# Performance work log

Measured on AMD Instinct MI355X. Metric: run time of the kernel, lower is better.

## Reference

```python
import jax, jax.numpy as jnp
import numpy as np

H, DN, DR, DV, L = 16, 128, 64, 128, 512
EPS = 1e-6

def rotate_half(x):
    x1, x2 = jnp.split(x, 2, axis=-1)
    return jnp.concatenate((-x2, x1), axis=-1)

def setup_inputs() -> dict:
    key = jax.random.key(0)
    ks = jax.random.split(key, 8)
    B, S, HID = 2, 2048, 2048
    inv_freq = 1.0 / (10000.0 ** (jnp.arange(0, DR, 2, dtype=jnp.float32) / DR))
    pos = jnp.arange(B * S, dtype=jnp.float32)
    freqs = pos[:, None] * inv_freq[None, :]
    emb = jnp.concatenate((freqs, freqs), axis=-1)
    return {
        "hidden_states": jax.random.normal(ks[0], (B, S, HID), jnp.float32),
        "cos": jnp.cos(emb),
        "sin": jnp.sin(emb),
        "q_proj_w": jax.random.normal(ks[1], (H * (DN + DR), HID), jnp.float32) * 0.02,
        "kv_a_proj_w": jax.random.normal(ks[2], (L + DR, HID), jnp.float32) * 0.02,
        "kv_a_ln_w": jnp.ones((L,), jnp.float32),
        "W_UK_T": jax.random.normal(ks[3], (H, DN, L), jnp.float32) * 0.02,
        "W_UV": jax.random.normal(ks[4], (H, L, DV), jnp.float32) * 0.02,
        "o_proj_w": jax.random.normal(ks[5], (HID, H * DV), jnp.float32) * 0.02,
    }

def reference(hidden_states, cos, sin, q_proj_w, kv_a_proj_w, kv_a_ln_w, W_UK_T, W_UV, o_proj_w):
    B, S, HID = hidden_states.shape
    T = B * S
    x = hidden_states.reshape(T, HID)
    # q projection -> [T, H, DN+DR]
    q = (x @ q_proj_w.T).reshape(T, H, DN + DR)
    q_pass, q_rot = q[..., :DN], q[..., DN:]
    # compressed kv -> latent + rope key (MQA-style, shared across heads)
    ckv = x @ kv_a_proj_w.T  # [T, L+DR]
    k_pass, k_rot = ckv[..., :L], ckv[..., L:]
    kv_c = k_pass * jax.lax.rsqrt(jnp.mean(k_pass * k_pass, axis=-1, keepdims=True) + EPS) * kv_a_ln_w
    # interleaved RoPE (rope_interleave=True): de-interleave then rotate_half form
    q_rot = q_rot.reshape(T, H, DR // 2, 2).swapaxes(-1, -2).reshape(T, H, DR)
    k_rot = k_rot.reshape(T, DR // 2, 2).swapaxes(-1, -2).reshape(T, DR)
    q_rot = q_rot * cos[:, None, :] + rotate_half(q_rot) * sin[:, None, :]
    k_rot = k_rot * cos + rotate_half(k_rot) * sin
    # absorb W_UK into queries: [T,H,L]
    q_lat = jnp.einsum('thd,hdl->thl', q_pass, W_UK_T)
    q_lat = q_lat.reshape(B, S, H, L)
    q_rot = q_rot.reshape(B, S, H, DR)
    kv_c_b = kv_c.reshape(B, S, L)
    k_rot_b = k_rot.reshape(B, S, DR)
    scale = 1.0 / np.sqrt(DN + DR)
    scores = (jnp.einsum('bshl,btl->bhst', q_lat, kv_c_b)
              + jnp.einsum('bshd,btd->bhst', q_rot, k_rot_b)) * scale
    causal = jnp.tril(jnp.ones((S, S), dtype=bool))
    scores = jnp.where(causal[None, None], scores, jnp.float32(-1e30))
    attn = jax.nn.softmax(scores, axis=-1)
    out_lat = jnp.einsum('bhst,btl->bshl', attn, kv_c_b)   # [B,S,H,L]
    out = jnp.einsum('bshl,hlv->bshv', out_lat, W_UV)       # [B,S,H,DV]
    out = out.reshape(B, S, H * DV) @ o_proj_w.T
    return out
```

## Files before the change

kernel.cpp:

```cpp
#include <hip/hip_runtime.h>
#include <stdint.h>

#define T_TOK 4096
#define HIDD  2048
#define NH    16
#define DNN   128
#define DRR   64
#define DVV   128
#define LAT   512
#define DQK   576
#define SEQ   2048
#define NB    2
#define KSTR  592
#define KCH   2368
#define QCKV  3712

typedef __attribute__((__ext_vector_type__(8))) short short8;
typedef __attribute__((__ext_vector_type__(4))) float f32x4;

__device__ __forceinline__ float bf2f(ushort u) {
  union { uint32_t i; float f; } v; v.i = ((uint32_t)u) << 16; return v.f;
}
__device__ __forceinline__ ushort f2bf(float f) {
  union { float f; uint32_t i; } v; v.f = f;
  uint32_t r = v.i + 0x7FFF + ((v.i >> 16) & 1);
  return (ushort)(r >> 16);
}

__device__ __forceinline__ void gld_lds16(const void* g, void* l) {
  __builtin_amdgcn_global_load_lds((const __attribute__((address_space(1))) void*)g,
                                   (__attribute__((address_space(3))) void*)l, 16, 0, 0);
}

__global__ void cast4(const float* __restrict__ in, ushort* __restrict__ out, int n4) {
  int i = blockIdx.x * blockDim.x + threadIdx.x;
  if (i >= n4) return;
  float4 v = ((const float4*)in)[i];
  ushort4 o; o.x = f2bf(v.x); o.y = f2bf(v.y); o.z = f2bf(v.z); o.w = f2bf(v.w);
  ((ushort4*)out)[i] = o;
}

__global__ void cast_pad_kv(const float* __restrict__ in, ushort* __restrict__ out) {
  int i = blockIdx.x * 256 + threadIdx.x;
  int row = (i * 4) >> 11;
  ushort4 o;
  if (row < 576) {
    float4 v = ((const float4*)in)[i];
    o.x = f2bf(v.x); o.y = f2bf(v.y); o.z = f2bf(v.z); o.w = f2bf(v.w);
  } else { o.x = 0; o.y = 0; o.z = 0; o.w = 0; }
  ((ushort4*)out)[i] = o;
}

__global__ void cast_wuk(const float* __restrict__ in, ushort* __restrict__ out) {
  int o = blockIdx.x * 256 + threadIdx.x;
  int d = o & 127, l = (o >> 7) & 511, h = o >> 16;
  out[o] = f2bf(in[((size_t)(h * 128 + d)) * 512 + l]);
}
__global__ void cast_wuv(const float* __restrict__ in, ushort* __restrict__ out) {
  int o = blockIdx.x * 256 + threadIdx.x;
  int l = o & 511, v = (o >> 9) & 127, h = o >> 16;
  out[o] = f2bf(in[((size_t)(h * 512 + l)) * 128 + v]);
}

template<int OUT_BF16>
__global__ __launch_bounds__(256) void gemm_bt(
    const ushort* __restrict__ A, const ushort* __restrict__ B, void* __restrict__ Cv,
    int K, int lda, int ldb, int ldc,
    long long aB, long long bB, long long cB)
{
  __shared__ ushort As[2][128 * 32];
  __shared__ ushort Bs[2][128 * 32];
  const int tid = threadIdx.x;
  const int lane = tid & 63, wid = tid >> 6;

  const int gx = gridDim.x;
  const int nwg = gx * gridDim.y;
  int l = blockIdx.y * gx + blockIdx.x;
  int tile = l;
  if ((nwg & 7) == 0) tile = (l & 7) * (nwg >> 3) + (l >> 3);
  const int m0 = (tile / gx) * 128, n0 = (tile % gx) * 128;

  A += (size_t)blockIdx.z * aB;
  B += (size_t)blockIdx.z * bB;
  const int wm = (wid >> 1) * 64, wn = (wid & 1) * 64;
  const int fr = lane & 15;
  const int kk = (lane >> 4) * 8;

  auto stage = [&](int k0, int buf) {
#pragma unroll
    for (int i = 0; i < 2; ++i) {
      int c = i * 256 + tid;
      gld_lds16(A + (size_t)(m0 + (c >> 2)) * lda + k0 + (c & 3) * 8, (void*)(&As[buf][0] + c * 8));
    }
#pragma unroll
    for (int i = 0; i < 2; ++i) {
      int c = i * 256 + tid;
      gld_lds16(B + (size_t)(n0 + (c >> 2)) * ldb + k0 + (c & 3) * 8, (void*)(&Bs[buf][0] + c * 8));
    }
  };

  f32x4 acc[4][4] = {};
  const int nt = K >> 5;
  stage(0, 0);
  for (int t = 0; t < nt; ++t) {
    const int cur = t & 1;
    if (t + 1 < nt) {
      stage((t + 1) << 5, cur ^ 1);
      asm volatile("s_waitcnt vmcnt(4)" ::: "memory");
    } else {
      asm volatile("s_waitcnt vmcnt(0)" ::: "memory");
    }
    __builtin_amdgcn_sched_barrier(0);
    __builtin_amdgcn_s_barrier();
    __builtin_amdgcn_sched_barrier(0);

    short8 af[4], bf[4];
#pragma unroll
    for (int x = 0; x < 4; ++x) af[x] = *(const short8*)(&As[cur][0] + (wm + x * 16 + fr) * 32 + kk);
#pragma unroll
    for (int x = 0; x < 4; ++x) bf[x] = *(const short8*)(&Bs[cur][0] + (wn + x * 16 + fr) * 32 + kk);
#pragma unroll
    for (int mi = 0; mi < 4; ++mi)
#pragma unroll
      for (int ni = 0; ni < 4; ++ni)
        acc[mi][ni] = __builtin_amdgcn_mfma_f32_16x16x32_bf16(af[mi], bf[ni], acc[mi][ni], 0, 0, 0);

    __builtin_amdgcn_sched_barrier(0);
    __builtin_amdgcn_s_barrier();
    __builtin_amdgcn_sched_barrier(0);
  }

  const int rb = (lane >> 4) * 4;
#pragma unroll
  for (int mi = 0; mi < 4; ++mi)
#pragma unroll
    for (int ni = 0; ni < 4; ++ni)
#pragma unroll
      for (int r = 0; r < 4; ++r) {
        size_t row = (size_t)(m0 + wm + mi * 16 + rb + r);
        size_t col = (size_t)(n0 + wn + ni * 16 + fr);
        size_t idx = row * (size_t)ldc + col + (size_t)blockIdx.z * cB;
        if (OUT_BF16) ((ushort*)Cv)[idx] = f2bf(acc[mi][ni][r]);
        else          ((float*)Cv)[idx]  = acc[mi][ni][r];
      }
}

__global__ __launch_bounds__(256) void rms_rope_k(
    const ushort* __restrict__ qckv, const float* __restrict__ lnw,
    const float* __restrict__ cosb, const float* __restrict__ sinb,
    ushort* __restrict__ k_eff)
{
  const int t = blockIdx.x, tid = threadIdx.x;
  __shared__ float red[4];
  const size_t base = (size_t)t * QCKV + 3072;
  float v0 = bf2f(qckv[base + tid]);
  float v1 = bf2f(qckv[base + 256 + tid]);
  float ss = v0 * v0 + v1 * v1;
#pragma unroll
  for (int m = 1; m < 64; m <<= 1) ss += __shfl_xor(ss, m);
  if ((tid & 63) == 0) red[tid >> 6] = ss;
  __syncthreads();
  float rn = rsqrtf((red[0] + red[1] + red[2] + red[3]) * (1.0f / 512.0f) + 1e-6f);
  k_eff[(size_t)t * KSTR + tid]       = f2bf(v0 * rn * lnw[tid]);
  k_eff[(size_t)t * KSTR + 256 + tid] = f2bf(v1 * rn * lnw[256 + tid]);
  if (tid < 64) {
    int j = tid;
    int src  = (j < 32) ? 2 * j : 2 * (j - 32) + 1;
    int psrc = (j < 32) ? src + 1 : src - 1;
    float xv = bf2f(qckv[base + 512 + src]);
    float pv = bf2f(qckv[base + 512 + psrc]);
    float c = cosb[t * 64 + j], s = sinb[t * 64 + j];
    k_eff[(size_t)t * KSTR + 512 + j] = f2bf((j < 32) ? xv * c - pv * s : xv * c + pv * s);
  }
}

__global__ __launch_bounds__(256) void transpose_kv(
    const ushort* __restrict__ keff, ushort* __restrict__ kvT)
{
  __shared__ ushort Tl[64][72];
  const int s0 = blockIdx.x * 64, v0 = blockIdx.y * 64, b = blockIdx.z;
  const int tid = threadIdx.x;
#pragma unroll
  for (int i = 0; i < 2; ++i) {
    int c = i * 256 + tid;
    int r = c >> 3, c8 = (c & 7) * 8;
    *(short8*)&Tl[r][c8] = *(const short8*)&keff[((size_t)b * SEQ + s0 + r) * KSTR + v0 + c8];
  }
  __syncthreads();
#pragma unroll
  for (int i = 0; i < 2; ++i) {
    int c = i * 256 + tid;
    int v = c >> 3, s8 = (c & 7) * 8;
    short8 o;
#pragma unroll
    for (int e = 0; e < 8; ++e) o[e] = Tl[s8 + e][v];
    *(short8*)&kvT[((size_t)b * 512 + v0 + v) * SEQ + s0 + s8] = o;
  }
}

__global__ void rope_q(const ushort* __restrict__ qb, const float* __restrict__ cosb,
                       const float* __restrict__ sinb, ushort* __restrict__ q_eff)
{
  const int t = blockIdx.x;
  const int h = blockIdx.y * 4 + threadIdx.y;
  const int j = threadIdx.x;
  size_t base = (size_t)t * QCKV + h * 192 + 128;
  int src  = (j < 32) ? 2 * j : 2 * (j - 32) + 1;
  int psrc = (j < 32) ? src + 1 : src - 1;
  float xv = bf2f(qb[base + src]), pv = bf2f(qb[base + psrc]);
  float c = cosb[t * 64 + j], s = sinb[t * 64 + j];
  q_eff[((size_t)h * T_TOK + t) * DQK + 512 + j] = f2bf((j < 32) ? xv * c - pv * s : xv * c + pv * s);
}

__global__ __launch_bounds__(512, 2) void attn3(
    const ushort* __restrict__ q_eff, const ushort* __restrict__ keff,
    const ushort* __restrict__ kvT, ushort* __restrict__ out_lat)
{
  const int pair = blockIdx.x;
  const int h = blockIdx.y, b = blockIdx.z;
  const int tid = threadIdx.x, lane = tid & 63, w = tid >> 6;
  __shared__ ushort Ks[2][32 * KSTR];
  __shared__ ushort Vt[2][512 * 32];
  __shared__ ushort Pl[8][16 * 40];

  const int fr = lane & 15, g = lane >> 4;

  auto stageK = [&](int kt, int buf) {
    const ushort* ksrc = keff + ((size_t)b * SEQ + (size_t)kt * 32) * KSTR;
    ushort* kd = &Ks[buf][0];
#pragma unroll
    for (int i = 0; i < 5; ++i) {
      int c0 = w * 320 + i * 64;
      if (c0 < KCH) {
        int c = c0 + lane;
        gld_lds16(ksrc + (size_t)c * 8, (void*)(kd + (size_t)c * 8));
      }
    }
  };
  auto stageV = [&](int kt, int buf) {
    const ushort* vsrc = kvT + (size_t)b * 512 * SEQ + (size_t)kt * 32;
    ushort* vd = &Vt[buf][0];
#pragma unroll
    for (int i = 0; i < 4; ++i) {
      int c = w * 256 + i * 64 + lane;
      gld_lds16(vsrc + (size_t)(c >> 2) * SEQ + (c & 3) * 8, (void*)(vd + (size_t)c * 8));
    }
  };

  for (int half = 0; half < 2; ++half) {
    const int qb = half ? pair : (15 - pair);
    const int q0 = qb * 128 + w * 16;

    const ushort* qrow = q_eff + ((size_t)h * T_TOK + (size_t)b * SEQ + q0 + fr) * DQK + g * 8;
    short8 qf[18];
#pragma unroll
    for (int ks = 0; ks < 18; ++ks) qf[ks] = *(const short8*)(qrow + ks * 32);

    f32x4 acc[32] = {};
    float m_s[4] = {-1e30f, -1e30f, -1e30f, -1e30f};
    float l_s[4] = {0.f, 0.f, 0.f, 0.f};

    const int nt = 4 * qb + 4;

    stageK(0, 0);
    stageV(0, 0);

    for (int kt = 0; kt < nt; ++kt) {
      const int cur = kt & 1;
      if (kt + 1 < nt) {
        stageK(kt + 1, cur ^ 1);
        stageV(kt + 1, cur ^ 1);
        if (w == 7) asm volatile("s_waitcnt vmcnt(6)" ::: "memory");
        else        asm volatile("s_waitcnt vmcnt(9)" ::: "memory");
      } else {
        asm volatile("s_waitcnt vmcnt(0)" ::: "memory");
      }
      __builtin_amdgcn_sched_barrier(0);
      __builtin_amdgcn_s_barrier();
      __builtin_amdgcn_sched_barrier(0);

      if (kt * 32 <= q0 + 15) {
        const ushort* Kc = &Ks[cur][0];
        const ushort* Vc = &Vt[cur][0];
        f32x4 s0 = {}, s1 = {};
        __builtin_amdgcn_s_setprio(1);
#pragma unroll
        for (int ks = 0; ks < 18; ++ks) {
          short8 b0 = *(const short8*)(Kc + (0 * 16 + fr) * KSTR + ks * 32 + g * 8);
          short8 b1 = *(const short8*)(Kc + (1 * 16 + fr) * KSTR + ks * 32 + g * 8);
          s0 = __builtin_amdgcn_mfma_f32_16x16x32_bf16(qf[ks], b0, s0, 0, 0, 0);
          s1 = __builtin_amdgcn_mfma_f32_16x16x32_bf16(qf[ks], b1, s1, 0, 0, 0);
        }
        __builtin_amdgcn_s_setprio(0);
        const float SC = 0.07216878364870322f;
        const bool diag = (kt * 32 + 31 > q0);
        float sv0[4], sv1[4];
#pragma unroll
        for (int r = 0; r < 4; ++r) {
          int qg = q0 + 4 * g + r;
          float a0 = s0[r] * SC, a1 = s1[r] * SC;
          if (diag) {
            if (kt * 32 + fr > qg)      a0 = -1e30f;
            if (kt * 32 + 16 + fr > qg) a1 = -1e30f;
          }
          sv0[r] = a0; sv1[r] = a1;
        }
        float mx[4];
#pragma unroll
        for (int r = 0; r < 4; ++r) {
          float m2 = fmaxf(sv0[r], sv1[r]);
          m2 = fmaxf(m2, __shfl_xor(m2, 1));
          m2 = fmaxf(m2, __shfl_xor(m2, 2));
          m2 = fmaxf(m2, __shfl_xor(m2, 4));
          m2 = fmaxf(m2, __shfl_xor(m2, 8));
          mx[r] = m2;
        }
        float need = mx[0] - m_s[0];
#pragma unroll
        for (int r = 1; r < 4; ++r) need = fmaxf(need, mx[r] - m_s[r]);
        if (__any(need > 8.0f)) {
          float rsc[4];
#pragma unroll
          for (int r = 0; r < 4; ++r) {
            float mn = fmaxf(m_s[r], mx[r]);
            rsc[r] = __expf(m_s[r] - mn);
            m_s[r] = mn;
            l_s[r] *= rsc[r];
          }
#pragma unroll
          for (int n2 = 0; n2 < 32; ++n2)
#pragma unroll
            for (int r = 0; r < 4; ++r) acc[n2][r] *= rsc[r];
        }
        float p0[4], p1[4];
#pragma unroll
        for (int r = 0; r < 4; ++r) {
          p0[r] = __expf(sv0[r] - m_s[r]);
          p1[r] = __expf(sv1[r] - m_s[r]);
          float ps = p0[r] + p1[r];
          ps += __shfl_xor(ps, 1);
          ps += __shfl_xor(ps, 2);
          ps += __shfl_xor(ps, 4);
          ps += __shfl_xor(ps, 8);
          l_s[r] += ps;
          Pl[w][(4 * g + r) * 40 + fr]      = f2bf(p0[r]);
          Pl[w][(4 * g + r) * 40 + 16 + fr] = f2bf(p1[r]);
        }
        short8 pa = *(const short8*)(Pl[w] + fr * 40 + g * 8);
        __builtin_amdgcn_s_setprio(1);
#pragma unroll
        for (int n2 = 0; n2 < 32; ++n2) {
          short8 bv = *(const short8*)(Vc + (n2 * 16 + fr) * 32 + g * 8);
          acc[n2] = __builtin_amdgcn_mfma_f32_16x16x32_bf16(pa, bv, acc[n2], 0, 0, 0);
        }
        __builtin_amdgcn_s_setprio(0);
      }
      __builtin_amdgcn_sched_barrier(0);
      __builtin_amdgcn_s_barrier();
      __builtin_amdgcn_sched_barrier(0);
    }

    const size_t obase = ((size_t)h * T_TOK + (size_t)b * SEQ + q0) * LAT;
    float inv[4];
#pragma unroll
    for (int r = 0; r < 4; ++r) inv[r] = 1.0f / l_s[r];
#pragma unroll
    for (int n2 = 0; n2 < 32; ++n2)
#pragma unroll
      for (int r = 0; r < 4; ++r)
        out_lat[obase + (size_t)(4 * g + r) * LAT + n2 * 16 + fr] = f2bf(acc[n2][r] * inv[r]);
  }
}

extern "C" void kernel_launch(void* const* d_in, const int* in_sizes, int n_in,
                              void* d_out, int out_size, void* d_ws, size_t ws_size,
                              hipStream_t stream) {
  const float* hs   = (const float*)d_in[0];
  const float* cosb = (const float*)d_in[1];
  const float* sinb = (const float*)d_in[2];
  const float* qw   = (const float*)d_in[3];
  const float* kvw  = (const float*)d_in[4];
  const float* lnw  = (const float*)d_in[5];
  const float* wuk  = (const float*)d_in[6];
  const float* wuv  = (const float*)d_in[7];
  const float* wo   = (const float*)d_in[8];
  float* out = (float*)d_out;
  char* ws = (char*)d_ws;

  const size_t o_xb   = 0;
  const size_t o_qb   = 16777216;
  const size_t o_wq   = 47185920;
  const size_t o_wkv  = 59768832;
  const size_t o_ol   = 0;
  const size_t o_wukt = 67108864;
  const size_t o_wuvt = 69206016;
  const size_t o_wo   = 71303168;
  const size_t o_keff = 79691776;
  const size_t o_qeff = 84541440;
  const size_t o_oh   = 160038912;
  const size_t o_kvt  = 176816128;

  ushort* xb    = (ushort*)(ws + o_xb);
  ushort* qbuf  = (ushort*)(ws + o_qb);
  ushort* wq_b  = (ushort*)(ws + o_wq);
  ushort* wkv_b = (ushort*)(ws + o_wkv);
  ushort* olat  = (ushort*)(ws + o_ol);
  ushort* wukt  = (ushort*)(ws + o_wukt);
  ushort* wuvt  = (ushort*)(ws + o_wuvt);
  ushort* wo_b  = (ushort*)(ws + o_wo);
  ushort* keff  = (ushort*)(ws + o_keff);
  ushort* qeff  = (ushort*)(ws + o_qeff);
  ushort* ohead = (ushort*)(ws + o_oh);
  ushort* kvt   = (ushort*)(ws + o_kvt);

  cast4<<<8192, 256, 0, stream>>>(hs, xb, 8388608 / 4);
  cast4<<<6144, 256, 0, stream>>>(qw, wq_b, 6291456 / 4);
  cast_pad_kv<<<1280, 256, 0, stream>>>(kvw, wkv_b);
  cast4<<<4096, 256, 0, stream>>>(wo, wo_b, 4194304 / 4);
  cast_wuk<<<4096, 256, 0, stream>>>(wuk, wukt);
  cast_wuv<<<4096, 256, 0, stream>>>(wuv, wuvt);

  gemm_bt<1><<<dim3(29, 32, 1), 256, 0, stream>>>(xb, wq_b, qbuf, 2048, 2048, 2048, QCKV, 0, 0, 0);
  rms_rope_k<<<4096, 256, 0, stream>>>(qbuf, lnw, cosb, sinb, keff);
  transpose_kv<<<dim3(32, 8, 2), 256, 0, stream>>>(keff, kvt);
  rope_q<<<dim3(4096, 4, 1), dim3(64, 4, 1), 0, stream>>>(qbuf, cosb, sinb, qeff);
  gemm_bt<1><<<dim3(4, 32, 16), 256, 0, stream>>>(qbuf, wukt, qeff, 128, QCKV, 128, 576,
                                                  192LL, 65536LL, 2359296LL);
  attn3<<<dim3(8, 16, 2), 512, 0, stream>>>(qeff, keff, kvt, olat);
  gemm_bt<1><<<dim3(1, 32, 16), 256, 0, stream>>>(olat, wuvt, ohead, 512, 512, 512, 2048,
                                                  2097152LL, 65536LL, 128LL);
  gemm_bt<0><<<dim3(16, 32, 1), 256, 0, stream>>>(ohead, wo_b, out, 2048, 2048, 2048, 2048, 0, 0, 0);
}
```

Baseline: 625.5 us.

## Shrink attention tiles to 64 query rows and 16-key steps with 16x16x16 MFMA

The causal latent-attention kernel now uses 256-thread blocks that each cover 64 query rows instead of 128, and steps through keys 16 at a time instead of 32. This doubles the grid and halves shared memory per block. The P·V product switches to 16x16x16 bf16 MFMA, with a fallback macro chain, so it matches the 16-key tile. The aim is better occupancy and finer causal skipping, paid for with more K/V reloads, twice as many barriers per key, and a smaller K dimension per MFMA; staging also over-reads some padding past each 16-row K tile.

```diff
diff --git a/kernel.cpp b/kernel.cpp
--- a/kernel.cpp
+++ b/kernel.cpp
@@ -12,11 +12,23 @@
 #define SEQ   2048
 #define NB    2
 #define KSTR  592
-#define KCH   2368
 #define QCKV  3712
 
 typedef __attribute__((__ext_vector_type__(8))) short short8;
+typedef __attribute__((__ext_vector_type__(4))) short short4v;
 typedef __attribute__((__ext_vector_type__(4))) float f32x4;
+
+#if __has_builtin(__builtin_amdgcn_mfma_f32_16x16x16_bf16)
+#define MFMA16(a, b, c) __builtin_amdgcn_mfma_f32_16x16x16_bf16(a, b, c, 0, 0, 0)
+#elif __has_builtin(__builtin_amdgcn_mfma_f32_16x16x16bf16_1k)
+#define MFMA16(a, b, c) __builtin_amdgcn_mfma_f32_16x16x16bf16_1k(a, b, c, 0, 0, 0)
+#else
+__device__ __forceinline__ f32x4 mfma16_asm(short4v a, short4v b, f32x4 c) {
+  asm volatile("v_mfma_f32_16x16x16_bf16 %0, %1, %2, %0" : "+v"(c) : "v"(a), "v"(b));
+  return c;
+}
+#define MFMA16(a, b, c) mfma16_asm(a, b, c)
+#endif
 
 __device__ __forceinline__ float bf2f(ushort u) {
   union { uint32_t i; float f; } v; v.i = ((uint32_t)u) << 16; return v.f;
@@ -212,44 +224,41 @@
   q_eff[((size_t)h * T_TOK + t) * DQK + 512 + j] = f2bf((j < 32) ? xv * c - pv * s : xv * c + pv * s);
 }
 
-__global__ __launch_bounds__(512, 2) void attn3(
+__global__ __launch_bounds__(256, 2) void attn7(
     const ushort* __restrict__ q_eff, const ushort* __restrict__ keff,
     const ushort* __restrict__ kvT, ushort* __restrict__ out_lat)
 {
   const int pair = blockIdx.x;
   const int h = blockIdx.y, b = blockIdx.z;
   const int tid = threadIdx.x, lane = tid & 63, w = tid >> 6;
-  __shared__ ushort Ks[2][32 * KSTR];
-  __shared__ ushort Vt[2][512 * 32];
-  __shared__ ushort Pl[8][16 * 40];
+  __shared__ ushort Ks[2][16 * 640];
+  __shared__ ushort Vt[2][512 * 16];
+  __shared__ ushort Pl[4][16 * 24];
 
   const int fr = lane & 15, g = lane >> 4;
 
   auto stageK = [&](int kt, int buf) {
-    const ushort* ksrc = keff + ((size_t)b * SEQ + (size_t)kt * 32) * KSTR;
+    const ushort* ksrc = keff + ((size_t)b * SEQ + (size_t)kt * 16) * KSTR;
     ushort* kd = &Ks[buf][0];
 #pragma unroll
     for (int i = 0; i < 5; ++i) {
-      int c0 = w * 320 + i * 64;
-      if (c0 < KCH) {
-        int c = c0 + lane;
-        gld_lds16(ksrc + (size_t)c * 8, (void*)(kd + (size_t)c * 8));
-      }
+      int c = i * 256 + tid;
+      gld_lds16(ksrc + (size_t)c * 8, (void*)(kd + (size_t)c * 8));
     }
   };
   auto stageV = [&](int kt, int buf) {
-    const ushort* vsrc = kvT + (size_t)b * 512 * SEQ + (size_t)kt * 32;
+    const ushort* vsrc = kvT + (size_t)b * 512 * SEQ + (size_t)kt * 16;
     ushort* vd = &Vt[buf][0];
 #pragma unroll
     for (int i = 0; i < 4; ++i) {
-      int c = w * 256 + i * 64 + lane;
-      gld_lds16(vsrc + (size_t)(c >> 2) * SEQ + (c & 3) * 8, (void*)(vd + (size_t)c * 8));
+      int c = i * 256 + tid;
+      gld_lds16(vsrc + (size_t)(c >> 1) * SEQ + (c & 1) * 8, (void*)(vd + (size_t)c * 8));
     }
   };
 
   for (int half = 0; half < 2; ++half) {
-    const int qb = half ? pair : (15 - pair);
-    const int q0 = qb * 128 + w * 16;
+    const int qb = half ? pair : (31 - pair);
+    const int q0 = qb * 64 + w * 16;
 
     const ushort* qrow = q_eff + ((size_t)h * T_TOK + (size_t)b * SEQ + q0 + fr) * DQK + g * 8;
     short8 qf[18];
@@ -270,8 +279,7 @@
       if (kt + 1 < nt) {
         stageK(kt + 1, cur ^ 1);
         stageV(kt + 1, cur ^ 1);
-        if (w == 7) asm volatile("s_waitcnt vmcnt(6)" ::: "memory");
-        else        asm volatile("s_waitcnt vmcnt(9)" ::: "memory");
+        asm volatile("s_waitcnt vmcnt(9)" ::: "memory");
       } else {
         asm volatile("s_waitcnt vmcnt(0)" ::: "memory");
       }
@@ -279,36 +287,31 @@
       __builtin_amdgcn_s_barrier();
       __builtin_amdgcn_sched_barrier(0);
 
-      if (kt * 32 <= q0 + 15) {
+      if (kt * 16 <= q0 + 15) {
         const ushort* Kc = &Ks[cur][0];
         const ushort* Vc = &Vt[cur][0];
-        f32x4 s0 = {}, s1 = {};
+        f32x4 s0 = {};
         __builtin_amdgcn_s_setprio(1);
 #pragma unroll
         for (int ks = 0; ks < 18; ++ks) {
-          short8 b0 = *(const short8*)(Kc + (0 * 16 + fr) * KSTR + ks * 32 + g * 8);
-          short8 b1 = *(const short8*)(Kc + (1 * 16 + fr) * KSTR + ks * 32 + g * 8);
+          short8 b0 = *(const short8*)(Kc + fr * KSTR + ks * 32 + g * 8);
           s0 = __builtin_amdgcn_mfma_f32_16x16x32_bf16(qf[ks], b0, s0, 0, 0, 0);
-          s1 = __builtin_amdgcn_mfma_f32_16x16x32_bf16(qf[ks], b1, s1, 0, 0, 0);
         }
         __builtin_amdgcn_s_setprio(0);
         const float SC = 0.07216878364870322f;
-        const bool diag = (kt * 32 + 31 > q0);
-        float sv0[4], sv1[4];
+        const bool diag = (kt * 16 + 15 > q0);
+        float sv0[4];
 #pragma unroll
         for (int r = 0; r < 4; ++r) {
           int qg = q0 + 4 * g + r;
-          float a0 = s0[r] * SC, a1 = s1[r] * SC;
-          if (diag) {
-            if (kt * 32 + fr > qg)      a0 = -1e30f;
-            if (kt * 32 + 16 + fr > qg) a1 = -1e30f;
-          }
-          sv0[r] = a0; sv1[r] = a1;
+          float a0 = s0[r] * SC;
+          if (diag && (kt * 16 + fr > qg)) a0 = -1e30f;
+          sv0[r] = a0;
         }
         float mx[4];
 #pragma unroll
         for (int r = 0; r < 4; ++r) {
-          float m2 = fmaxf(sv0[r], sv1[r]);
+          float m2 = sv0[r];
           m2 = fmaxf(m2, __shfl_xor(m2, 1));
           m2 = fmaxf(m2, __shfl_xor(m2, 2));
           m2 = fmaxf(m2, __shfl_xor(m2, 4));
@@ -332,26 +335,24 @@
 #pragma unroll
             for (int r = 0; r < 4; ++r) acc[n2][r] *= rsc[r];
         }
-        float p0[4], p1[4];
+        float p0[4];
 #pragma unroll
         for (int r = 0; r < 4; ++r) {
           p0[r] = __expf(sv0[r] - m_s[r]);
-          p1[r] = __expf(sv1[r] - m_s[r]);
-          float ps = p0[r] + p1[r];
+          float ps = p0[r];
           ps += __shfl_xor(ps, 1);
           ps += __shfl_xor(ps, 2);
           ps += __shfl_xor(ps, 4);
           ps += __shfl_xor(ps, 8);
           l_s[r] += ps;
-          Pl[w][(4 * g + r) * 40 + fr]      = f2bf(p0[r]);
-          Pl[w][(4 * g + r) * 40 + 16 + fr] = f2bf(p1[r]);
-        }
-        short8 pa = *(const short8*)(Pl[w] + fr * 40 + g * 8);
+          Pl[w][(4 * g + r) * 24 + fr] = f2bf(p0[r]);
+        }
+        short4v pa = *(const short4v*)(Pl[w] + fr * 24 + g * 4);
         __builtin_amdgcn_s_setprio(1);
 #pragma unroll
         for (int n2 = 0; n2 < 32; ++n2) {
-          short8 bv = *(const short8*)(Vc + (n2 * 16 + fr) * 32 + g * 8);
-          acc[n2] = __builtin_amdgcn_mfma_f32_16x16x32_bf16(pa, bv, acc[n2], 0, 0, 0);
+          short4v bv = *(const short4v*)(Vc + (n2 * 16 + fr) * 16 + g * 4);
+          acc[n2] = MFMA16(pa, bv, acc[n2]);
         }
         __builtin_amdgcn_s_setprio(0);
       }
@@ -426,7 +427,7 @@
   rope_q<<<dim3(4096, 4, 1), dim3(64, 4, 1), 0, stream>>>(qbuf, cosb, sinb, qeff);
   gemm_bt<1><<<dim3(4, 32, 16), 256, 0, stream>>>(qbuf, wukt, qeff, 128, QCKV, 128, 576,
                                                   192LL, 65536LL, 2359296LL);
-  attn3<<<dim3(8, 16, 2), 512, 0, stream>>>(qeff, keff, kvt, olat);
+  attn7<<<dim3(16, 16, 2), 256, 0, stream>>>(qeff, keff, kvt, olat);
   gemm_bt<1><<<dim3(1, 32, 16), 256, 0, stream>>>(olat, wuvt, ohead, 512, 512, 512, 2048,
                                                   2097152LL, 65536LL, 128LL);
   gemm_bt<0><<<dim3(16, 32, 1), 256, 0, stream>>>(ohead, wo_b, out, 2048, 2048, 2048, 2048, 0, 0, 0);
```

Measured after the change: 733.0 us. 1.17x slower.
